# Performance work log

Measured on AMD Instinct MI355X. Metric: run time of the kernel, lower is better.

Reference implementation:

```python
import jax, jax.numpy as jnp
import numpy as np

DIM = 1024
HID = int(DIM * 1.5)  # 1536
K = 4


def setup_inputs() -> dict:
    key = jax.random.key(0)
    ks = jax.random.split(key, 8)
    N, T = 4, 2048
    x = jax.random.normal(ks[0], (N, T, DIM), dtype=jnp.float32)
    input_w = jax.random.normal(ks[1], (2 * HID, DIM), dtype=jnp.float32) * (1.0 / DIM ** 0.5)
    conv_w = jax.random.normal(ks[2], (HID, 1, K), dtype=jnp.float32) * (1.0 / K ** 0.5)
    conv_b = jnp.zeros((HID,), dtype=jnp.float32)
    gates_w = jax.random.normal(ks[3], (2 * HID, HID), dtype=jnp.float32) * (1.0 / HID ** 0.5)
    gates_b = jnp.zeros((2 * HID,), dtype=jnp.float32)
    forget_base = jnp.linspace(-6.7, -10.5, HID, dtype=jnp.float32)
    output_w = jax.random.normal(ks[4], (DIM, HID), dtype=jnp.float32) * (1.0 / HID ** 0.5)
    return {"x": x, "input_w": input_w, "conv_w": conv_w, "conv_b": conv_b,
            "gates_w": gates_w, "gates_b": gates_b, "forget_base": forget_base,
            "output_w": output_w}


def _hawk(x, input_w, conv_w, conv_b, gates_w, gates_b, forget_base, output_w):
    N, T, _ = x.shape
    gi = jnp.einsum('ntc,hc->nth', x, input_w)          # [N,T,2H]
    gate, xh = jnp.split(gi, 2, axis=-1)                # each [N,T,H]
    # causal depthwise conv1d (torch pads k-1 both sides then slices [:T])
    y = jax.lax.conv_general_dilated(
        xh.transpose(0, 2, 1), conv_w, window_strides=(1,),
        padding=[(K - 1, 0)], feature_group_count=HID,
        dimension_numbers=('NCH', 'OIH', 'NCH'))
    xh = (y + conv_b[None, :, None]).transpose(0, 2, 1)  # [N,T,H]
    fg = jnp.einsum('nth,gh->ntg', xh, gates_w) + gates_b
    forget, inp = jnp.split(fg, 2, axis=-1)
    log_alpha = -8.0 * jax.nn.softplus(forget_base) * jax.nn.sigmoid(forget)
    alpha = jnp.exp(log_alpha)
    beta = jnp.sqrt(1.0 - alpha ** 2)
    xi = beta * jax.nn.sigmoid(inp) * xh
    # linear recurrence h_t = alpha_t * h_{t-1} + xi_t via associative scan over T
    def combine(c1, c2):
        a1, b1 = c1
        a2, b2 = c2
        return a1 * a2, a2 * b1 + b2
    _, h = jax.lax.associative_scan(combine, (alpha, xi), axis=1)
    out = jnp.einsum('nth,dh->ntd', jax.nn.gelu(gate, approximate=False) * h, output_w)
    return out


def reference(x, input_w, conv_w, conv_b, gates_w, gates_b, forget_base, output_w):
    return _hawk(x, input_w, conv_w, conv_b, gates_w, gates_b, forget_base, output_w)
```

## Files before the change

### kernel.cpp

```cpp
#include <hip/hip_runtime.h>
#include <cstdint>
#include <cstddef>

typedef unsigned short u16;
typedef __attribute__((ext_vector_type(2))) unsigned short u16x2;
typedef __attribute__((ext_vector_type(4))) unsigned short u16x4;
typedef __attribute__((ext_vector_type(8))) short bf16x8;
typedef __attribute__((ext_vector_type(4))) float f32x4;

#define DIMC 1024
#define HIDC 1536
#define TT 2048
#define NN 4
#define NT 8192
#define CHUNK 32
#define NCH 64

__device__ inline u16 bf16r(float f) {
    unsigned int u = __float_as_uint(f);
    unsigned int r = (u + 0x7fffu + ((u >> 16) & 1u)) >> 16;
    return (u16)r;
}
__device__ inline float bf2f(u16 v) {
    return __uint_as_float(((unsigned int)v) << 16);
}

__device__ inline void gload_lds16(const u16* g, u16* l) {
    __builtin_amdgcn_global_load_lds(
        (const __attribute__((address_space(1))) void*)g,
        (__attribute__((address_space(3))) void*)l, 16, 0, 0);
}

__global__ __launch_bounds__(256) void cast4_kernel(const float* __restrict__ s0, u16* __restrict__ d0, int n0,
                                                    const float* __restrict__ s1, u16* __restrict__ d1, int n1,
                                                    const float* __restrict__ s2, u16* __restrict__ d2, int n2,
                                                    const float* __restrict__ s3, u16* __restrict__ d3, int n3) {
    int i = blockIdx.x * 256 + threadIdx.x;
    const float* s; u16* d; int j = i;
    if (j < n0) { s = s0; d = d0; }
    else {
        j -= n0;
        if (j < n1) { s = s1; d = d1; }
        else {
            j -= n1;
            if (j < n2) { s = s2; d = d2; }
            else {
                j -= n2;
                if (j >= n3) return;
                s = s3; d = d3;
            }
        }
    }
    float4 v = ((const float4*)s)[j];
    u16x4 o;
    o.x = bf16r(v.x); o.y = bf16r(v.y); o.z = bf16r(v.z); o.w = bf16r(v.w);
    *(u16x4*)&d[(size_t)j * 4] = o;
}

template<int BN_, int WM, int OUTF32>
__device__ __forceinline__ void gemm_body(const u16* __restrict__ A,
                                          const u16* __restrict__ B,
                                          int M, int N, int K,
                                          const float* __restrict__ bias,
                                          float* __restrict__ Cf,
                                          u16* __restrict__ out0,
                                          u16* __restrict__ out1,
                                          int nsplit, int w0, int w1) {
    constexpr int WN    = 8 / WM;
    constexpr int MF    = 16 / WM;
    constexpr int NFRAG = BN_ / (WN * 16);
    constexpr int NBL   = (BN_ * 4 + 511) / 512;
    constexpr int VNW   = 2 + NBL;
    constexpr int SA    = 8192;
    constexpr int SB    = BN_ * 32;

    extern __shared__ u16 lds[];
    const int tid  = threadIdx.x;
    const int lane = tid & 63;
    const int wv   = tid >> 6;
    const int rr   = lane & 15;
    const int clin = lane >> 4;
    const int wr = wv / WN, wc = wv % WN;

    const int nb  = N / BN_;
    const int nwg = gridDim.x;
    const int cpx = nwg >> 3;
    const int wg  = (blockIdx.x & 7) * cpx + (blockIdx.x >> 3);
    const int bm = wg / nb, bn = wg % nb;
    const int NTK = K >> 6;

    int offA[2], offB[NBL];
    #pragma unroll
    for (int r = 0; r < 2; r++) {
        int u = r * 512 + wv * 64 + lane;
        int R = u >> 2;
        int ch = (u & 3) ^ ((R >> 1) & 3);
        offA[r] = R * K + ch * 8;
    }
    #pragma unroll
    for (int r = 0; r < NBL; r++) {
        int wvr = (r == 0) ? wv : (wv & 3);
        int u = r * 512 + wvr * 64 + lane;
        int R = u >> 2;
        int ch = (u & 3) ^ ((R >> 1) & 3);
        offB[r] = R * K + ch * 8;
    }
    const u16* Abase = A + (size_t)(bm * 256) * K;
    const u16* Bbase = B + (size_t)(bn * BN_) * K;
    u16* ldsA = lds;
    u16* ldsB = lds + 4 * SA;

    const int coff = (clin ^ ((rr >> 1) & 3)) * 8;

    f32x4 acc[MF][NFRAG];
    #pragma unroll
    for (int m = 0; m < MF; m++)
        #pragma unroll
        for (int n = 0; n < NFRAG; n++)
            acc[m][n] = f32x4{0.f, 0.f, 0.f, 0.f};

#define STAGE_A(t, ks) do { \
    int _tc = (t) < NTK ? (t) : (NTK - 1); \
    const u16* _g = Abase + _tc * 64 + (ks) * 32; \
    u16* _sl = ldsA + (((t) & 1) * 2 + (ks)) * SA + wv * 512; \
    gload_lds16(_g + offA[0], _sl); \
    gload_lds16(_g + offA[1], _sl + 4096); } while (0)
#define STAGE_B(t, ks) do { \
    int _tc = (t) < NTK ? (t) : (NTK - 1); \
    const u16* _g = Bbase + _tc * 64 + (ks) * 32; \
    u16* _s0 = ldsB + (((t) & 1) * 2 + (ks)) * SB; \
    gload_lds16(_g + offB[0], _s0 + wv * 512); \
    if (NBL == 2) gload_lds16(_g + offB[1], _s0 + 4096 + (wv & 3) * 512); } while (0)
#define RD_A(buf, ks, m) (*(const bf16x8*)&ldsA[((buf) * 2 + (ks)) * SA + (wr * (MF * 16) + (m) * 16 + rr) * 32 + coff])
#define RD_B(buf, ks, n) (*(const bf16x8*)&ldsB[((buf) * 2 + (ks)) * SB + (wc * (NFRAG * 16) + (n) * 16 + rr) * 32 + coff])
#define MMA_ALL do { \
    __builtin_amdgcn_s_setprio(1); \
    _Pragma("unroll") \
    for (int _i = 0; _i < MF; _i++) \
        _Pragma("unroll") \
        for (int _j = 0; _j < NFRAG; _j++) \
            acc[_i][_j] = __builtin_amdgcn_mfma_f32_16x16x32_bf16(af[_i], bfr[_j], acc[_i][_j], 0, 0, 0); \
    __builtin_amdgcn_s_setprio(0); } while (0)
#define PHASE_TAIL(WAITVM) do { \
    asm volatile("s_waitcnt lgkmcnt(0)" ::: "memory"); \
    if (WAITVM) asm volatile("s_waitcnt vmcnt(%0)" :: "i"(VNW) : "memory"); \
    __builtin_amdgcn_s_barrier(); \
    asm volatile("" ::: "memory"); } while (0)

    STAGE_A(0, 0); STAGE_B(0, 0); STAGE_A(0, 1); STAGE_B(0, 1);
    STAGE_A(1, 0); STAGE_B(1, 0);
    asm volatile("s_waitcnt vmcnt(%0)" :: "i"(VNW) : "memory");
    __builtin_amdgcn_s_barrier();
    asm volatile("" ::: "memory");

    bf16x8 af[MF];
    bf16x8 bfr[NFRAG];
    for (int t = 0; t < NTK; ++t) {
        const int buf = t & 1;
        STAGE_A(t + 1, 1); STAGE_B(t + 1, 1);
        #pragma unroll
        for (int i = 0; i < MF; i++) af[i] = RD_A(buf, 0, i);
        #pragma unroll
        for (int j = 0; j < NFRAG; j++) bfr[j] = RD_B(buf, 0, j);
        MMA_ALL;
        PHASE_TAIL(0);
        STAGE_A(t + 2, 0); STAGE_B(t + 2, 0);
        #pragma unroll
        for (int i = 0; i < MF; i++) af[i] = RD_A(buf, 1, i);
        #pragma unroll
        for (int j = 0; j < NFRAG; j++) bfr[j] = RD_B(buf, 1, j);
        MMA_ALL;
        PHASE_TAIL(1);
    }

    asm volatile("s_waitcnt vmcnt(0)" ::: "memory");
    __builtin_amdgcn_s_barrier();
    asm volatile("" ::: "memory");
    const int colg = bn * BN_ + wc * (NFRAG * 16);
    const int row0 = bm * 256 + wr * (MF * 16);
    float bv[NFRAG];
    #pragma unroll
    for (int n = 0; n < NFRAG; n++) bv[n] = bias ? bias[colg + n * 16 + rr] : 0.f;

    if (OUTF32) {
        #pragma unroll
        for (int n = 0; n < NFRAG; n++) {
            int col = colg + n * 16 + rr;
            #pragma unroll
            for (int m = 0; m < MF; m++) {
                int rbase = row0 + m * 16 + clin * 4;
                #pragma unroll
                for (int r = 0; r < 4; r++)
                    Cf[(size_t)(rbase + r) * N + col] = acc[m][n][r] + bv[n];
            }
        }
    } else {
        u16* wreg = lds + wv * 4096;
        u16* dst; int nout, cd;
        if (colg < nsplit) { dst = out0; nout = w0; cd = colg; }
        else               { dst = out1; nout = w1; cd = colg - nsplit; }
        #pragma unroll
        for (int p = 0; p < NFRAG / 2; p++) {
            #pragma unroll
            for (int m = 0; m < MF; m++)
                #pragma unroll
                for (int nn = 0; nn < 2; nn++) {
                    int f = 2 * p + nn;
                    #pragma unroll
                    for (int r = 0; r < 4; r++)
                        wreg[(m * 16 + clin * 4 + r) * 32 + nn * 16 + rr] =
                            bf16r(acc[m][f][r] + bv[f]);
                }
            asm volatile("s_waitcnt lgkmcnt(0)" ::: "memory");
            __builtin_amdgcn_sched_barrier(0);
            #pragma unroll
            for (int j = 0; j < MF; j++) {
                int lr = j * 16 + (lane >> 2);
                int lc = (lane & 3) * 8;
                bf16x8 v = *(const bf16x8*)&wreg[lr * 32 + lc];
                *(bf16x8*)&dst[(size_t)(row0 + lr) * nout + cd + p * 32 + lc] = v;
            }
            asm volatile("s_waitcnt lgkmcnt(0)" ::: "memory");
            __builtin_amdgcn_sched_barrier(0);
        }
    }
#undef STAGE_A
#undef STAGE_B
#undef RD_A
#undef RD_B
#undef MMA_ALL
#undef PHASE_TAIL
}

__global__ __launch_bounds__(512, 2) void gemm_in(const u16* A, const u16* B, int M, int N, int K,
                                                  const float* bias, u16* o0, u16* o1,
                                                  int nsplit, int w0, int w1) {
    gemm_body<192, 4, 0>(A, B, M, N, K, bias, nullptr, o0, o1, nsplit, w0, w1);
}
__global__ __launch_bounds__(512, 2) void gemm_gates(const u16* A, const u16* B, int M, int N, int K,
                                                     const float* bias, u16* o0, u16* o1,
                                                     int nsplit, int w0, int w1) {
    gemm_body<192, 4, 0>(A, B, M, N, K, bias, nullptr, o0, o1, nsplit, w0, w1);
}
__global__ __launch_bounds__(512, 2) void gemm_out(const u16* A, const u16* B, int M, int N, int K,
                                                   const float* bias, float* Cf, u16* o0, u16* o1,
                                                   int nsplit, int w0, int w1) {
    gemm_body<128, 2, 1>(A, B, M, N, K, bias, Cf, o0, o1, nsplit, w0, w1);
}

__global__ __launch_bounds__(256) void conv_kernel(const u16* __restrict__ xhb,
                                                   const float* __restrict__ cw,
                                                   const float* __restrict__ cb,
                                                   u16* __restrict__ xcb) {
    int idx = blockIdx.x * 256 + threadIdx.x;
    int hb = idx % (HIDC / 8);
    int tg = idx / (HIDC / 8);
    int t0 = (tg & (TT / 8 - 1)) * 8;
    int n  = tg / (TT / 8);
    int h0 = hb * 8;

    float w[4][8], bias[8];
    #pragma unroll
    for (int j = 0; j < 8; j++) {
        bias[j] = cb[h0 + j];
        float4 wv4 = *(const float4*)&cw[(h0 + j) * 4];
        w[0][j] = wv4.x; w[1][j] = wv4.y; w[2][j] = wv4.z; w[3][j] = wv4.w;
    }

    const u16* base = xhb + ((size_t)(n * TT + t0)) * HIDC + h0;
    u16* outp = xcb + ((size_t)(n * TT + t0)) * HIDC + h0;

    float xm0[8], xm1[8], xm2[8], cur[8];
    #pragma unroll
    for (int j = 0; j < 8; j++) { xm0[j] = 0.f; xm1[j] = 0.f; xm2[j] = 0.f; }
    if (t0 >= 3) {
        bf16x8 v = *(const bf16x8*)(base - 3 * HIDC);
        #pragma unroll
        for (int j = 0; j < 8; j++) xm0[j] = bf2f((u16)v[j]);
    }
    if (t0 >= 2) {
        bf16x8 v = *(const bf16x8*)(base - 2 * HIDC);
        #pragma unroll
        for (int j = 0; j < 8; j++) xm1[j] = bf2f((u16)v[j]);
    }
    if (t0 >= 1) {
        bf16x8 v = *(const bf16x8*)(base - 1 * HIDC);
        #pragma unroll
        for (int j = 0; j < 8; j++) xm2[j] = bf2f((u16)v[j]);
    }

    #pragma unroll
    for (int s = 0; s < 8; s++) {
        bf16x8 v = *(const bf16x8*)(base + s * HIDC);
        #pragma unroll
        for (int j = 0; j < 8; j++) cur[j] = bf2f((u16)v[j]);
        bf16x8 o;
        #pragma unroll
        for (int j = 0; j < 8; j++) {
            float acc = bias[j] + w[3][j] * cur[j] + w[2][j] * xm2[j]
                      + w[1][j] * xm1[j] + w[0][j] * xm0[j];
            o[j] = (short)bf16r(acc);
        }
        *(bf16x8*)(outp + s * HIDC) = o;
        #pragma unroll
        for (int j = 0; j < 8; j++) { xm0[j] = xm1[j]; xm1[j] = xm2[j]; xm2[j] = cur[j]; }
    }
}

__device__ inline void alpha_xi(u16 f, u16 i, u16 x, float s, float& a, float& xi) {
    float la = s / (1.f + __expf(-bf2f(f)));
    a = 1.f + la * (1.f + 0.5f * la);
    float b2 = fmaxf(0.f, 1.f - a * a);
    xi = sqrtf(b2) * (1.f / (1.f + __expf(-bf2f(i)))) * bf2f(x);
}

__global__ __launch_bounds__(256) void scan1_kernel(const u16* __restrict__ fgb,
                                                    const u16* __restrict__ xcb,
                                                    const float* __restrict__ fb,
                                                    float* __restrict__ Ac,
                                                    float* __restrict__ Bc) {
    int idx = blockIdx.x * 256 + threadIdx.x;
    int hb = idx % (HIDC / 2);
    int c  = (idx / (HIDC / 2)) % NCH;
    int n  = idx / ((HIDC / 2) * NCH);
    int h0 = hb * 2;
    float s0 = -8.f * log1pf(__expf(fb[h0]));
    float s1 = -8.f * log1pf(__expf(fb[h0 + 1]));
    const u16* pf = fgb + ((size_t)(n * TT + c * CHUNK)) * (2 * HIDC) + h0;
    const u16* px = xcb + ((size_t)(n * TT + c * CHUNK)) * HIDC + h0;
    float A0 = 1.f, B0 = 0.f, A1 = 1.f, B1 = 0.f;
    #pragma unroll 4
    for (int t = 0; t < CHUNK; t++) {
        u16x2 f2 = *(const u16x2*)pf;
        u16x2 i2 = *(const u16x2*)(pf + HIDC);
        u16x2 x2 = *(const u16x2*)px;
        float a, xi;
        alpha_xi(f2.x, i2.x, x2.x, s0, a, xi);
        A0 *= a; B0 = a * B0 + xi;
        alpha_xi(f2.y, i2.y, x2.y, s1, a, xi);
        A1 *= a; B1 = a * B1 + xi;
        pf += 2 * HIDC; px += HIDC;
    }
    size_t o = ((size_t)(n * NCH + c)) * HIDC + h0;
    Ac[o] = A0; Ac[o + 1] = A1;
    Bc[o] = B0; Bc[o + 1] = B1;
}

__global__ __launch_bounds__(256) void scan3_kernel(const u16* __restrict__ fgb,
                                                    const u16* __restrict__ xcb,
                                                    const u16* __restrict__ gateb,
                                                    const float* __restrict__ fb,
                                                    const float* __restrict__ Ac,
                                                    const float* __restrict__ Bc,
                                                    u16* __restrict__ gb) {
    int idx = blockIdx.x * 256 + threadIdx.x;
    int hb = idx % (HIDC / 2);
    int c  = (idx / (HIDC / 2)) % NCH;
    int n  = idx / ((HIDC / 2) * NCH);
    int h0 = hb * 2;
    float s0 = -8.f * log1pf(__expf(fb[h0]));
    float s1 = -8.f * log1pf(__expf(fb[h0 + 1]));
    float h0v = 0.f, h1v = 0.f;
    #pragma unroll 4
    for (int cc = 0; cc < c; cc++) {
        size_t j = ((size_t)(n * NCH + cc)) * HIDC + h0;
        h0v = Ac[j] * h0v + Bc[j];
        h1v = Ac[j + 1] * h1v + Bc[j + 1];
    }
    const u16* pf = fgb + ((size_t)(n * TT + c * CHUNK)) * (2 * HIDC) + h0;
    const u16* px = xcb + ((size_t)(n * TT + c * CHUNK)) * HIDC + h0;
    const u16* pg = gateb + ((size_t)(n * TT + c * CHUNK)) * HIDC + h0;
    u16* po = gb + ((size_t)(n * TT + c * CHUNK)) * HIDC + h0;
    #pragma unroll 4
    for (int t = 0; t < CHUNK; t++) {
        u16x2 f2 = *(const u16x2*)pf;
        u16x2 i2 = *(const u16x2*)(pf + HIDC);
        u16x2 x2 = *(const u16x2*)px;
        u16x2 g2 = *(const u16x2*)pg;
        float a, xi;
        alpha_xi(f2.x, i2.x, x2.x, s0, a, xi);
        h0v = a * h0v + xi;
        alpha_xi(f2.y, i2.y, x2.y, s1, a, xi);
        h1v = a * h1v + xi;
        float g0 = bf2f(g2.x), g1 = bf2f(g2.y);
        float gl0 = 0.5f * g0 * (1.f + erff(g0 * 0.70710678118654752f));
        float gl1 = 0.5f * g1 * (1.f + erff(g1 * 0.70710678118654752f));
        u16x2 ov;
        ov.x = bf16r(gl0 * h0v);
        ov.y = bf16r(gl1 * h1v);
        *(u16x2*)po = ov;
        pf += 2 * HIDC; px += HIDC; pg += HIDC; po += HIDC;
    }
}

extern "C" void kernel_launch(void* const* d_in, const int* in_sizes, int n_in,
                              void* d_out, int out_size, void* d_ws, size_t ws_size,
                              hipStream_t stream) {
    const float* x           = (const float*)d_in[0];
    const float* input_w     = (const float*)d_in[1];
    const float* conv_w      = (const float*)d_in[2];
    const float* conv_b      = (const float*)d_in[3];
    const float* gates_w     = (const float*)d_in[4];
    const float* gates_b     = (const float*)d_in[5];
    const float* forget_base = (const float*)d_in[6];
    const float* output_w    = (const float*)d_in[7];
    float* out = (float*)d_out;

    size_t off = 0;
    char* wsb = (char*)d_ws;
    auto alloc = [&](size_t bytes) { char* p = wsb + off; off += bytes; return p; };
    u16* w1b   = (u16*)alloc((size_t)3072 * DIMC * 2);
    u16* w2b   = (u16*)alloc((size_t)3072 * HIDC * 2);
    u16* w3b   = (u16*)alloc((size_t)DIMC * HIDC * 2);
    u16* xbf   = (u16*)alloc((size_t)NT * DIMC * 2);
    u16* gateb = (u16*)alloc((size_t)NT * HIDC * 2);
    u16* xhb   = (u16*)alloc((size_t)NT * HIDC * 2);
    u16* xcb   = (u16*)alloc((size_t)NT * HIDC * 2);
    u16* fgb   = (u16*)alloc((size_t)NT * 2 * HIDC * 2);
    if (off > ws_size) return;

    float* Ac    = (float*)xbf;
    float* Bc    = Ac + (size_t)NN * NCH * HIDC;
    u16* gb = xhb;

    (void)hipFuncSetAttribute((const void*)&gemm_in,
                              hipFuncAttributeMaxDynamicSharedMemorySize, 114688);
    (void)hipFuncSetAttribute((const void*)&gemm_gates,
                              hipFuncAttributeMaxDynamicSharedMemorySize, 114688);
    (void)hipFuncSetAttribute((const void*)&gemm_out,
                              hipFuncAttributeMaxDynamicSharedMemorySize, 98304);

    const int n0 = NT * DIMC / 4;
    const int n1 = 3072 * DIMC / 4;
    const int n2 = 3072 * HIDC / 4;
    const int n3 = DIMC * HIDC / 4;
    cast4_kernel<<<(n0 + n1 + n2 + n3) / 256, 256, 0, stream>>>(
        x, xbf, n0, input_w, w1b, n1, gates_w, w2b, n2, output_w, w3b, n3);

    gemm_in<<<(NT / 256) * (3072 / 192), 512, 114688, stream>>>(
        xbf, w1b, NT, 3072, DIMC, nullptr, gateb, xhb, HIDC, HIDC, HIDC);

    conv_kernel<<<(NT / 8) * (HIDC / 8) / 256, 256, 0, stream>>>(xhb, conv_w, conv_b, xcb);

    gemm_gates<<<(NT / 256) * (3072 / 192), 512, 114688, stream>>>(
        xcb, w2b, NT, 3072, HIDC, gates_b, fgb, nullptr, 3072, 3072, 3072);

    scan1_kernel<<<NN * NCH * (HIDC / 2) / 256, 256, 0, stream>>>(fgb, xcb, forget_base, Ac, Bc);
    scan3_kernel<<<NN * NCH * (HIDC / 2) / 256, 256, 0, stream>>>(fgb, xcb, gateb, forget_base, Ac, Bc, gb);

    gemm_out<<<(NT / 256) * (DIMC / 128), 512, 98304, stream>>>(
        gb, w3b, NT, DIMC, HIDC, nullptr, out, nullptr, nullptr, 0, 0, 0);
}
```

Measured before the change: 264.3 us.

## Fuse causal depthwise conv into input GEMM epilogue with boundary fixup kernel

The causal depthwise conv is now computed inside the input-projection GEMM epilogue, reading neighbouring rows from the per-wave LDS staging tile, and the xh half is written straight to the convolved buffer. Rows at 64-row tile edges (first 3) lack their predecessors, so raw values for boundary rows are saved and a small fixup kernel recomputes those rows. This drops the full conv pass, which read and wrote the whole xh tensor. In exchange the GEMM epilogue gets extra LDS reads, weight loads and a second boundary store path.

```diff
diff --git a/kernel.cpp b/kernel.cpp
--- a/kernel.cpp
+++ b/kernel.cpp
@@ -57,7 +57,7 @@
     *(u16x4*)&d[(size_t)j * 4] = o;
 }
 
-template<int BN_, int WM, int OUTF32>
+template<int BN_, int WM, int OUTF32, int CONV>
 __device__ __forceinline__ void gemm_body(const u16* __restrict__ A,
                                           const u16* __restrict__ B,
                                           int M, int N, int K,
@@ -65,7 +65,10 @@
                                           float* __restrict__ Cf,
                                           u16* __restrict__ out0,
                                           u16* __restrict__ out1,
-                                          int nsplit, int w0, int w1) {
+                                          int nsplit, int w0, int w1,
+                                          const float* __restrict__ cw,
+                                          const float* __restrict__ cb,
+                                          u16* __restrict__ rawb) {
     constexpr int WN    = 8 / WM;
     constexpr int MF    = 16 / WM;
     constexpr int NFRAG = BN_ / (WN * 16);
@@ -197,8 +200,11 @@
     } else {
         u16* wreg = lds + wv * 4096;
         u16* dst; int nout, cd;
-        if (colg < nsplit) { dst = out0; nout = w0; cd = colg; }
-        else               { dst = out1; nout = w1; cd = colg - nsplit; }
+        const bool half1 = (colg >= nsplit);
+        if (!half1) { dst = out0; nout = w0; cd = colg; }
+        else        { dst = out1; nout = w1; cd = colg - nsplit; }
+        const bool doconv = CONV && half1;
+        const int lr = 0;  (void)lr;
         #pragma unroll
         for (int p = 0; p < NFRAG / 2; p++) {
             #pragma unroll
@@ -213,12 +219,48 @@
                 }
             asm volatile("s_waitcnt lgkmcnt(0)" ::: "memory");
             __builtin_amdgcn_sched_barrier(0);
-            #pragma unroll
-            for (int j = 0; j < MF; j++) {
-                int lr = j * 16 + (lane >> 2);
+            if (!doconv) {
+                #pragma unroll
+                for (int j = 0; j < MF; j++) {
+                    int r_ = j * 16 + (lane >> 2);
+                    int lc = (lane & 3) * 8;
+                    bf16x8 v = *(const bf16x8*)&wreg[r_ * 32 + lc];
+                    *(bf16x8*)&dst[(size_t)(row0 + r_) * nout + cd + p * 32 + lc] = v;
+                }
+            } else {
                 int lc = (lane & 3) * 8;
-                bf16x8 v = *(const bf16x8*)&wreg[lr * 32 + lc];
-                *(bf16x8*)&dst[(size_t)(row0 + lr) * nout + cd + p * 32 + lc] = v;
+                int ch0 = cd + p * 32 + lc;
+                float w4[4][8], bb[8];
+                #pragma unroll
+                for (int jj = 0; jj < 8; jj++) {
+                    bb[jj] = cb[ch0 + jj];
+                    float4 wv4 = *(const float4*)&cw[(ch0 + jj) * 4];
+                    w4[0][jj] = wv4.x; w4[1][jj] = wv4.y; w4[2][jj] = wv4.z; w4[3][jj] = wv4.w;
+                }
+                #pragma unroll
+                for (int j = 0; j < MF; j++) {
+                    int r_ = j * 16 + (lane >> 2);
+                    bf16x8 v0 = *(const bf16x8*)&wreg[r_ * 32 + lc];
+                    if (r_ >= 3) {
+                        bf16x8 v1 = *(const bf16x8*)&wreg[(r_ - 1) * 32 + lc];
+                        bf16x8 v2 = *(const bf16x8*)&wreg[(r_ - 2) * 32 + lc];
+                        bf16x8 v3 = *(const bf16x8*)&wreg[(r_ - 3) * 32 + lc];
+                        bf16x8 o;
+                        #pragma unroll
+                        for (int jj = 0; jj < 8; jj++) {
+                            float a = bb[jj] + w4[3][jj] * bf2f((u16)v0[jj])
+                                            + w4[2][jj] * bf2f((u16)v1[jj])
+                                            + w4[1][jj] * bf2f((u16)v2[jj])
+                                            + w4[0][jj] * bf2f((u16)v3[jj]);
+                            o[jj] = (short)bf16r(a);
+                        }
+                        *(bf16x8*)&dst[(size_t)(row0 + r_) * nout + ch0] = o;
+                    } else {
+                        *(bf16x8*)&rawb[(size_t)(row0 + r_) * nout + ch0] = v0;
+                    }
+                    if (r_ >= 61)
+                        *(bf16x8*)&rawb[(size_t)(row0 + r_) * nout + ch0] = v0;
+                }
             }
             asm volatile("s_waitcnt lgkmcnt(0)" ::: "memory");
             __builtin_amdgcn_sched_barrier(0);
@@ -234,77 +276,48 @@
 
 __global__ __launch_bounds__(512, 2) void gemm_in(const u16* A, const u16* B, int M, int N, int K,
                                                   const float* bias, u16* o0, u16* o1,
-                                                  int nsplit, int w0, int w1) {
-    gemm_body<192, 4, 0>(A, B, M, N, K, bias, nullptr, o0, o1, nsplit, w0, w1);
+                                                  int nsplit, int w0, int w1,
+                                                  const float* cw, const float* cb, u16* rawb) {
+    gemm_body<192, 4, 0, 1>(A, B, M, N, K, bias, nullptr, o0, o1, nsplit, w0, w1, cw, cb, rawb);
 }
 __global__ __launch_bounds__(512, 2) void gemm_gates(const u16* A, const u16* B, int M, int N, int K,
                                                      const float* bias, u16* o0, u16* o1,
                                                      int nsplit, int w0, int w1) {
-    gemm_body<192, 4, 0>(A, B, M, N, K, bias, nullptr, o0, o1, nsplit, w0, w1);
+    gemm_body<192, 4, 0, 0>(A, B, M, N, K, bias, nullptr, o0, o1, nsplit, w0, w1, nullptr, nullptr, nullptr);
 }
 __global__ __launch_bounds__(512, 2) void gemm_out(const u16* A, const u16* B, int M, int N, int K,
                                                    const float* bias, float* Cf, u16* o0, u16* o1,
                                                    int nsplit, int w0, int w1) {
-    gemm_body<128, 2, 1>(A, B, M, N, K, bias, Cf, o0, o1, nsplit, w0, w1);
-}
-
-__global__ __launch_bounds__(256) void conv_kernel(const u16* __restrict__ xhb,
-                                                   const float* __restrict__ cw,
-                                                   const float* __restrict__ cb,
-                                                   u16* __restrict__ xcb) {
+    gemm_body<128, 2, 1, 0>(A, B, M, N, K, bias, Cf, o0, o1, nsplit, w0, w1, nullptr, nullptr, nullptr);
+}
+
+__global__ __launch_bounds__(256) void convfix_kernel(const u16* __restrict__ xhb,
+                                                      const float* __restrict__ cw,
+                                                      const float* __restrict__ cb,
+                                                      u16* __restrict__ xcb) {
     int idx = blockIdx.x * 256 + threadIdx.x;
     int hb = idx % (HIDC / 8);
-    int tg = idx / (HIDC / 8);
-    int t0 = (tg & (TT / 8 - 1)) * 8;
-    int n  = tg / (TT / 8);
+    int rg = idx / (HIDC / 8);
+    int nt = (rg / 3) * 64 + (rg % 3);
+    int t = nt & (TT - 1);
     int h0 = hb * 8;
-
-    float w[4][8], bias[8];
-    #pragma unroll
-    for (int j = 0; j < 8; j++) {
-        bias[j] = cb[h0 + j];
-        float4 wv4 = *(const float4*)&cw[(h0 + j) * 4];
-        w[0][j] = wv4.x; w[1][j] = wv4.y; w[2][j] = wv4.z; w[3][j] = wv4.w;
-    }
-
-    const u16* base = xhb + ((size_t)(n * TT + t0)) * HIDC + h0;
-    u16* outp = xcb + ((size_t)(n * TT + t0)) * HIDC + h0;
-
-    float xm0[8], xm1[8], xm2[8], cur[8];
-    #pragma unroll
-    for (int j = 0; j < 8; j++) { xm0[j] = 0.f; xm1[j] = 0.f; xm2[j] = 0.f; }
-    if (t0 >= 3) {
-        bf16x8 v = *(const bf16x8*)(base - 3 * HIDC);
-        #pragma unroll
-        for (int j = 0; j < 8; j++) xm0[j] = bf2f((u16)v[j]);
-    }
-    if (t0 >= 2) {
-        bf16x8 v = *(const bf16x8*)(base - 2 * HIDC);
-        #pragma unroll
-        for (int j = 0; j < 8; j++) xm1[j] = bf2f((u16)v[j]);
-    }
-    if (t0 >= 1) {
-        bf16x8 v = *(const bf16x8*)(base - 1 * HIDC);
-        #pragma unroll
-        for (int j = 0; j < 8; j++) xm2[j] = bf2f((u16)v[j]);
-    }
-
-    #pragma unroll
-    for (int s = 0; s < 8; s++) {
-        bf16x8 v = *(const bf16x8*)(base + s * HIDC);
-        #pragma unroll
-        for (int j = 0; j < 8; j++) cur[j] = bf2f((u16)v[j]);
-        bf16x8 o;
-        #pragma unroll
-        for (int j = 0; j < 8; j++) {
-            float acc = bias[j] + w[3][j] * cur[j] + w[2][j] * xm2[j]
-                      + w[1][j] * xm1[j] + w[0][j] * xm0[j];
-            o[j] = (short)bf16r(acc);
+    float acc[8];
+    #pragma unroll
+    for (int j = 0; j < 8; j++) acc[j] = cb[h0 + j];
+    #pragma unroll
+    for (int k = 0; k < 4; k++) {
+        int d = 3 - k;
+        if (t >= d) {
+            bf16x8 v = *(const bf16x8*)&xhb[(size_t)(nt - d) * HIDC + h0];
+            #pragma unroll
+            for (int j = 0; j < 8; j++)
+                acc[j] += bf2f((u16)v[j]) * cw[(h0 + j) * 4 + k];
         }
-        *(bf16x8*)(outp + s * HIDC) = o;
-        #pragma unroll
-        for (int j = 0; j < 8; j++) { xm0[j] = xm1[j]; xm1[j] = xm2[j]; xm2[j] = cur[j]; }
-    }
+    }
+    bf16x8 o;
+    #pragma unroll
+    for (int j = 0; j < 8; j++) o[j] = (short)bf16r(acc[j]);
+    *(bf16x8*)&xcb[(size_t)nt * HIDC + h0] = o;
 }
 
 __device__ inline void alpha_xi(u16 f, u16 i, u16 x, float s, float& a, float& xi) {
@@ -438,9 +451,11 @@
         x, xbf, n0, input_w, w1b, n1, gates_w, w2b, n2, output_w, w3b, n3);
 
     gemm_in<<<(NT / 256) * (3072 / 192), 512, 114688, stream>>>(
-        xbf, w1b, NT, 3072, DIMC, nullptr, gateb, xhb, HIDC, HIDC, HIDC);
-
-    conv_kernel<<<(NT / 8) * (HIDC / 8) / 256, 256, 0, stream>>>(xhb, conv_w, conv_b, xcb);
+        xbf, w1b, NT, 3072, DIMC, nullptr, gateb, xcb, HIDC, HIDC, HIDC,
+        conv_w, conv_b, xhb);
+
+    convfix_kernel<<<(NT / 64) * 3 * (HIDC / 8) / 256, 256, 0, stream>>>(
+        xhb, conv_w, conv_b, xcb);
 
     gemm_gates<<<(NT / 256) * (3072 / 192), 512, 114688, stream>>>(
         xcb, w2b, NT, 3072, HIDC, gates_b, fgb, nullptr, 3072, 3072, 3072);
```

Result: slower. 275.0 us (+4.0%).
